# Optimization experiments

Hardware: AMD Instinct MI355X
Metric: run time of the kernel (lower is better)

The kernel has to match this reference:

```python
import jax, jax.numpy as jnp
import numpy as np

S, L, D, H = 4, 2048, 1024, 16
DH = D // H
W_CLUSTER = 384
ROUTING_ITERS = 1
TTOT = S * L


def setup_inputs() -> dict:
    key = jax.random.key(0)
    ks = jax.random.split(key, 8)
    scale = 1.0 / np.sqrt(D)
    return {
        "q_in": jax.random.normal(ks[0], (TTOT, D), jnp.float32),
        "k_in": jax.random.normal(ks[1], (TTOT, D), jnp.float32),
        "v_in": jax.random.normal(ks[2], (TTOT, D), jnp.float32),
        "seqlens_tokens": jnp.full((S,), L, jnp.int32),
        "global_idx_per_set": jax.random.randint(ks[3], (S,), 0, TTOT),
        "Wq": jax.random.normal(ks[4], (D, D), jnp.float32) * scale,
        "Wk": jax.random.normal(ks[5], (D, D), jnp.float32) * scale,
        "Wv": jax.random.normal(ks[6], (D, D), jnp.float32) * scale,
        "Wo": jax.random.normal(ks[7], (D, D), jnp.float32) * scale,
    }


def _l2n(x, eps=1e-6):
    return x / (jnp.linalg.norm(x, axis=-1, keepdims=True) + eps)


def _route_np(r, lens, gidx, w, iters):
    # Host-side per-sequence k-means routing (mirrors the original host-sync loop).
    # Returns augmented token order (global token appended per cluster) and cluster lens.
    bounds = np.concatenate([[0], np.cumsum(lens)])
    order_chunks, len_chunks = [], []
    for s in range(len(lens)):
        a, b = int(bounds[s]), int(bounds[s + 1])
        Ls = b - a
        if Ls <= 0:
            continue
        feats = r[a:b]
        wloc = max(1, min(w, Ls))
        k = max(1, (Ls + wloc - 1) // wloc)
        init_idx = np.clip(np.round(np.linspace(0.0, max(Ls - 1, 0), k)).astype(np.int64), 0, Ls - 1)
        cent = feats[init_idx]
        for _ in range(max(1, iters)):
            sims = feats @ cent.T
            assign = sims.argmax(1)
            sums = np.zeros_like(cent)
            np.add.at(sums, assign, feats)
            counts = np.bincount(assign, minlength=k).astype(cent.dtype)
            cent = sums / np.maximum(counts, 1.0)[:, None]
            cent = cent / (np.linalg.norm(cent, axis=-1, keepdims=True) + 1e-6)
        sims = feats @ cent.T
        assign = sims.argmax(1)
        own = sims[np.arange(Ls), assign]
        order1 = np.argsort(-own, kind="stable")
        assign1 = assign[order1]
        order2 = np.argsort(assign1, kind="stable")
        perm = order1[order2]
        cid = assign1[order2]
        counts = np.bincount(cid, minlength=k)
        keep = np.minimum(counts, wloc)
        starts = np.cumsum(counts) - counts
        pos = np.arange(Ls) - np.repeat(starts, counts)
        keep_mask = pos < keep[cid]
        kept = perm[keep_mask] + a  # absolute kept token indices, cluster-sorted
        kc = keep[keep > 0]
        C = kc.size
        ins = np.cumsum(kc) + np.arange(C)  # insertion slot after each cluster
        total = int(kc.sum()) + C
        wg = np.empty(total, dtype=np.int64)
        m = np.ones(total, dtype=bool)
        m[ins] = False
        wg[m] = kept
        wg[~m] = int(gidx[s])
        order_chunks.append(wg)
        len_chunks.append((kc + 1).astype(np.int64))
    return np.concatenate(order_chunks), np.concatenate(len_chunks)


def _padded_indices(order, lens):
    Ncl, Lmax = lens.size, int(lens.max())
    valid = np.arange(Lmax)[None, :] < lens[:, None]
    idx = np.zeros((Ncl, Lmax), dtype=np.int64)
    idx[valid] = order  # row-major fill matches per-cluster concat order
    return idx, valid


def _attend_and_merge(qh, kh, vh, idx, mask):
    # Padded-varlen non-causal attention per cluster, then mean-merge duplicates.
    scale = 1.0 / np.sqrt(DH)
    qg, kg, vg = qh[idx], kh[idx], vh[idx]  # [Ncl, Lmax, H, Dh]
    scores = jnp.einsum("clhd,cmhd->chlm", qg, kg) * scale
    scores = jnp.where(mask[:, None, None, :], scores, -1e9)
    attn = jax.nn.softmax(scores, axis=-1)
    out = jnp.einsum("chlm,cmhd->clhd", attn, vg)
    out = out * mask[:, :, None, None]
    out_h = jnp.zeros((TTOT, H, DH), out.dtype).at[idx].add(out)
    cnt = jnp.zeros((TTOT,), out.dtype).at[idx].add(mask.astype(out.dtype))
    return out_h / jnp.clip(cnt, 1.0)[:, None, None]


def reference(q_in, k_in, v_in, seqlens_tokens, global_idx_per_set, Wq, Wk, Wv, Wo):
    qh = (q_in @ Wq.T).reshape(TTOT, H, DH)
    kh = (k_in @ Wk.T).reshape(TTOT, H, DH)
    vh = (v_in @ Wv.T).reshape(TTOT, H, DH)
    r = 0.5 * (_l2n(qh.mean(1)) + _l2n(kh.mean(1)))  # routing features (detached in original)
    order, lens = _route_np(np.asarray(r), np.asarray(seqlens_tokens),
                            np.asarray(global_idx_per_set), W_CLUSTER, ROUTING_ITERS)
    idx_np, valid_np = _padded_indices(order, lens)
    idx, mask = jnp.asarray(idx_np), jnp.asarray(valid_np)
    out_h = _attend_and_merge(qh, kh, vh, idx, mask)
    return out_h.reshape(TTOT, D) @ Wo.T
```

## Files before the change

kernel.cpp:

```cpp
#include <hip/hip_runtime.h>
#include <math.h>

#define S_ 4
#define L_ 2048
#define D_ 1024
#define H_ 16
#define DH_ 64
#define TTOT_ 8192
#define WCL_ 384
#define KMAX_ 16
#define MAXCL_ (S_*KMAX_)
#define MAXLEN_ (WCL_+1)
#define LSCAP_ 4096
#define NELEM_ ((size_t)TTOT_*(size_t)D_)

typedef __attribute__((ext_vector_type(8))) short bf16x8;
typedef __attribute__((ext_vector_type(4))) float f32x4;
typedef __attribute__((ext_vector_type(4))) unsigned short u16x4;

__device__ __forceinline__ unsigned short bfh(float x) {
  unsigned u = __float_as_uint(x);
  return (unsigned short)((u + 0x7FFFu + ((u >> 16) & 1u)) >> 16);
}
__device__ __forceinline__ float bff(unsigned short h) {
  return __uint_as_float(((unsigned)h) << 16);
}
__device__ __forceinline__ unsigned pk2(unsigned short a, unsigned short b) {
  return (unsigned)a | ((unsigned)b << 16);
}
#define SWZ(r, c) (((r) << 6) + ((c) ^ (((r) & 7) << 3)))

__device__ __forceinline__ void glds16(const void* g, void* l) {
  __builtin_amdgcn_global_load_lds(
      (const __attribute__((address_space(1))) unsigned int*)g,
      (__attribute__((address_space(3))) unsigned int*)l, 16, 0, 0);
}

#define N4W_ ((1 << 20) / 4)
#define N4IN_ ((int)(NELEM_ / 4))
#define NWM_ (64 * 1024)

__global__ __launch_bounds__(256)
void wmean2(const float* __restrict__ Wq, const float* __restrict__ Wk,
            float* __restrict__ Wqm, float* __restrict__ Wkm) {
  const float* __restrict__ W = blockIdx.y ? Wk : Wq;
  float* __restrict__ Wm = blockIdx.y ? Wkm : Wqm;
  int i = blockIdx.x * 256 + threadIdx.x;
  if (i >= NWM_) return;
  int d = i >> 10, kk = i & 1023;
  float s = 0.f;
#pragma unroll
  for (int h = 0; h < 16; h++) s += W[(size_t)(h * 64 + d) * 1024 + kk];
  Wm[i] = s * (1.0f / 16.0f);
}

__global__ __launch_bounds__(256)
void feats_conv(const float* __restrict__ q_in, const float* __restrict__ k_in,
                const float* __restrict__ v_in,
                const float* __restrict__ Wqm, const float* __restrict__ Wkm,
                float* __restrict__ FQ, float* __restrict__ FK,
                const float* __restrict__ Wq, const float* __restrict__ Wk,
                const float* __restrict__ Wv, const float* __restrict__ Wo,
                unsigned short* __restrict__ WqH, unsigned short* __restrict__ WkH,
                unsigned short* __restrict__ WvH, unsigned short* __restrict__ WoH,
                unsigned short* __restrict__ QSh, unsigned short* __restrict__ KSh,
                unsigned short* __restrict__ VSh) {
  if (blockIdx.x < 256) {
    const int by = blockIdx.x >> 7;
    const float* __restrict__ A = by ? k_in : q_in;
    const float* __restrict__ B = by ? Wkm : Wqm;
    float* __restrict__ C = by ? FK : FQ;
    const int Kd = 1024, N = 64;
    __shared__ float As[16][68];
    __shared__ float Bs[16][68];
    const int tx = threadIdx.x & 15, ty = threadIdx.x >> 4;
    const int m0 = (blockIdx.x & 127) * 64;
    const int lr = threadIdx.x >> 2, lc = threadIdx.x & 3;
    float acc[4][4] = {};
    for (int k0 = 0; k0 < Kd; k0 += 16) {
      __syncthreads();
      float4 a4 = *(const float4*)(A + (size_t)(m0 + lr) * Kd + k0 + lc * 4);
      float4 b4 = *(const float4*)(B + (size_t)lr * Kd + k0 + lc * 4);
      As[lc*4+0][lr] = a4.x; As[lc*4+1][lr] = a4.y; As[lc*4+2][lr] = a4.z; As[lc*4+3][lr] = a4.w;
      Bs[lc*4+0][lr] = b4.x; Bs[lc*4+1][lr] = b4.y; Bs[lc*4+2][lr] = b4.z; Bs[lc*4+3][lr] = b4.w;
      __syncthreads();
#pragma unroll
      for (int kk = 0; kk < 16; kk++) {
        float4 av = *(const float4*)&As[kk][ty * 4];
        float4 bv = *(const float4*)&Bs[kk][tx * 4];
        float aa[4] = {av.x, av.y, av.z, av.w};
        float bb[4] = {bv.x, bv.y, bv.z, bv.w};
#pragma unroll
        for (int i = 0; i < 4; i++)
#pragma unroll
          for (int j = 0; j < 4; j++) acc[i][j] += aa[i] * bb[j];
      }
    }
#pragma unroll
    for (int i = 0; i < 4; i++)
#pragma unroll
      for (int j = 0; j < 4; j++)
        C[(size_t)(m0 + ty * 4 + i) * N + (tx * 4 + j)] = acc[i][j];
    return;
  }
  int i = (blockIdx.x - 256) * 256 + threadIdx.x;
  if (i < 4 * N4W_) {
    int w = i / N4W_, j = i % N4W_;
    const float* src = (w == 0) ? Wq : (w == 1) ? Wk : (w == 2) ? Wv : Wo;
    unsigned short* dst = (w == 0) ? WqH : (w == 1) ? WkH : (w == 2) ? WvH : WoH;
    float4 v = ((const float4*)src)[j];
    *(uint2*)&dst[(size_t)j * 4] =
        make_uint2(pk2(bfh(v.x), bfh(v.y)), pk2(bfh(v.z), bfh(v.w)));
    return;
  }
  i -= 4 * N4W_;
  if (i >= 3 * N4IN_) return;
  int w = i / N4IN_, j = i % N4IN_;
  const float* src = (w == 0) ? q_in : (w == 1) ? k_in : v_in;
  unsigned short* dh = (w == 0) ? QSh : (w == 1) ? KSh : VSh;
  float4 v = ((const float4*)src)[j];
  *(uint2*)&dh[(size_t)j * 4] =
      make_uint2(pk2(bfh(v.x), bfh(v.y)), pk2(bfh(v.z), bfh(v.w)));
}

__device__ __forceinline__
void gemm1_body(const unsigned short* __restrict__ Ah,
                const unsigned short* __restrict__ Bh,
                unsigned short* __restrict__ Ch,
                int b, unsigned char* smem) {
  const int Kd = D_, N = D_;
  const int m0 = (b & 63) * 128, n0 = (b >> 6) * 128;
  unsigned short* LA = (unsigned short*)smem;
  unsigned short* LB = LA + 8192;
  const int tid = threadIdx.x, wave = tid >> 6, lane = tid & 63;
  const int lm = lane & 15, lg = lane >> 4;
  const int wr = wave >> 1, wc = wave & 1;
  const int lrow = lane >> 3;
  const int lchk = (lane & 7) ^ lrow;
  f32x4 acc[4][4];
#pragma unroll
  for (int i = 0; i < 4; i++)
#pragma unroll
    for (int j = 0; j < 4; j++) acc[i][j] = (f32x4){0.f, 0.f, 0.f, 0.f};
  for (int k0 = 0; k0 < Kd; k0 += 64) {
    __syncthreads();
#pragma unroll
    for (int i = 0; i < 4; i++) {
      const int r = wave * 32 + i * 8;
      const size_t ga = (size_t)(m0 + r + lrow) * Kd + k0 + lchk * 8;
      const size_t gb = (size_t)(n0 + r + lrow) * Kd + k0 + lchk * 8;
      glds16(&Ah[ga], &LA[r * 64]);
      glds16(&Bh[gb], &LB[r * 64]);
    }
    __syncthreads();
#pragma unroll
    for (int s = 0; s < 2; s++) {
      bf16x8 ah[4], bh[4];
#pragma unroll
      for (int i = 0; i < 4; i++) {
        const int ra = wr * 64 + i * 16 + lm;
        const int ca = ((s * 4 + lg) ^ (ra & 7)) * 8;
        ah[i] = *(const bf16x8*)&LA[ra * 64 + ca];
        const int rb = wc * 64 + i * 16 + lm;
        const int cb = ((s * 4 + lg) ^ (rb & 7)) * 8;
        bh[i] = *(const bf16x8*)&LB[rb * 64 + cb];
      }
#pragma unroll
      for (int i = 0; i < 4; i++)
#pragma unroll
        for (int j = 0; j < 4; j++)
          acc[i][j] = __builtin_amdgcn_mfma_f32_16x16x32_bf16(ah[i], bh[j], acc[i][j], 0, 0, 0);
    }
  }
#pragma unroll
  for (int i = 0; i < 4; i++)
#pragma unroll
    for (int j = 0; j < 4; j++) {
      const int rowb = m0 + wr * 64 + i * 16 + lg * 4;
      const int col = n0 + wc * 64 + j * 16 + lm;
#pragma unroll
      for (int r = 0; r < 4; r++)
        Ch[(size_t)(rowb + r) * N + col] = bfh(acc[i][j][r]);
    }
}

__global__ __launch_bounds__(256)
void gemm_o1(const unsigned short* __restrict__ Ah,
             const unsigned short* __restrict__ Bh,
             float* __restrict__ C) {
  __shared__ __align__(16) unsigned short LA[128 * 64];
  __shared__ __align__(16) unsigned short LB[128 * 64];
  const int Kd = D_, N = D_;
  const int tid = threadIdx.x, wave = tid >> 6, lane = tid & 63;
  const int lm = lane & 15, lg = lane >> 4;
  const int m0 = (blockIdx.x & 63) * 128, n0 = (blockIdx.x >> 6) * 128;
  const int wr = wave >> 1, wc = wave & 1;
  const int lrow = lane >> 3;
  const int lchk = (lane & 7) ^ lrow;
  f32x4 acc[4][4];
#pragma unroll
  for (int i = 0; i < 4; i++)
#pragma unroll
    for (int j = 0; j < 4; j++) acc[i][j] = (f32x4){0.f, 0.f, 0.f, 0.f};
  for (int k0 = 0; k0 < Kd; k0 += 64) {
    __syncthreads();
#pragma unroll
    for (int i = 0; i < 4; i++) {
      const int r = wave * 32 + i * 8;
      const size_t ga = (size_t)(m0 + r + lrow) * Kd + k0 + lchk * 8;
      const size_t gb = (size_t)(n0 + r + lrow) * Kd + k0 + lchk * 8;
      glds16(&Ah[ga], &LA[r * 64]);
      glds16(&Bh[gb], &LB[r * 64]);
    }
    __syncthreads();
#pragma unroll
    for (int s = 0; s < 2; s++) {
      bf16x8 ah[4], bh[4];
#pragma unroll
      for (int i = 0; i < 4; i++) {
        const int ra = wr * 64 + i * 16 + lm;
        const int ca = ((s * 4 + lg) ^ (ra & 7)) * 8;
        ah[i] = *(const bf16x8*)&LA[ra * 64 + ca];
        const int rb = wc * 64 + i * 16 + lm;
        const int cb = ((s * 4 + lg) ^ (rb & 7)) * 8;
        bh[i] = *(const bf16x8*)&LB[rb * 64 + cb];
      }
#pragma unroll
      for (int i = 0; i < 4; i++)
#pragma unroll
        for (int j = 0; j < 4; j++)
          acc[i][j] = __builtin_amdgcn_mfma_f32_16x16x32_bf16(ah[i], bh[j], acc[i][j], 0, 0, 0);
    }
  }
#pragma unroll
  for (int i = 0; i < 4; i++)
#pragma unroll
    for (int j = 0; j < 4; j++) {
      const int rowb = m0 + wr * 64 + i * 16 + lg * 4;
      const int col = n0 + wc * 64 + j * 16 + lm;
#pragma unroll
      for (int r = 0; r < 4; r++)
        C[(size_t)(rowb + r) * N + col] = acc[i][j][r];
    }
}

__global__ __launch_bounds__(256)
void l2comb(const float* __restrict__ FQ, const float* __restrict__ FK,
            float* __restrict__ FE) {
  int t = blockIdx.x * 4 + (threadIdx.x >> 6);
  int lane = threadIdx.x & 63;
  if (t >= TTOT_) return;
  float q = FQ[(size_t)t * 64 + lane], k = FK[(size_t)t * 64 + lane];
  float q2 = q * q, k2 = k * k;
#pragma unroll
  for (int m = 1; m < 64; m <<= 1) {
    q2 += __shfl_xor(q2, m, 64);
    k2 += __shfl_xor(k2, m, 64);
  }
  FE[(size_t)t * 64 + lane] =
      0.5f * (q / (sqrtf(q2) + 1e-6f) + k / (sqrtf(k2) + 1e-6f));
}

__device__ void routing_body(int s, const float* __restrict__ FE,
                             const int* __restrict__ seqlens,
                             const int* __restrict__ gidx, int* __restrict__ cT,
                             int* __restrict__ cL, int* __restrict__ tC,
                             unsigned char* smem) {
  __builtin_amdgcn_s_setprio(1);
  unsigned long long* keys = (unsigned long long*)smem;
  unsigned char* assign = smem + 32768;
  float (*cent)[64] = (float(*)[64])(smem + 36864);
  int* cnt1 = (int*)(smem + 40960);
  int* cnt2 = cnt1 + KMAX_;
  int* starts = cnt2 + KMAX_;
  float* fstage = (float*)smem;

  const int tid = threadIdx.x;
  int a = 0;
  for (int t = 0; t < s; t++) a += seqlens[t];
  int Ls = seqlens[s];
  if (Ls > LSCAP_) Ls = LSCAP_;
  for (int cs = tid; cs < KMAX_; cs += 1024) cL[s * KMAX_ + cs] = 0;
  if (Ls <= 0) return;

  int wloc = Ls < WCL_ ? Ls : WCL_;
  if (wloc < 1) wloc = 1;
  int k = (Ls + wloc - 1) / wloc;
  if (k < 1) k = 1;
  if (k > KMAX_) k = KMAX_;

  if (tid < k * 64) {
    int j = tid >> 6, d = tid & 63;
    double step = (k > 1) ? (double)(Ls - 1) / (double)(k - 1) : 0.0;
    long ii = (long)rint(step * (double)j);
    if (ii < 0) ii = 0;
    if (ii > Ls - 1) ii = Ls - 1;
    cent[j][d] = FE[(size_t)(a + ii) * DH_ + d];
  }
  if (tid < KMAX_) { cnt1[tid] = 0; cnt2[tid] = 0; }
  __syncthreads();

  for (int base2 = 0; base2 < Ls; base2 += 1024) {
    int i = base2 + tid;
    int aj = -1;
    if (i < Ls) {
      const float4* f4 = (const float4*)(FE + (size_t)(a + i) * DH_);
      float4 fr[16];
#pragma unroll
      for (int c4 = 0; c4 < 16; c4++) fr[c4] = f4[c4];
      float best = -1e30f; int bj = 0;
      for (int j = 0; j < k; j++) {
        float sd = 0.f;
#pragma unroll
        for (int c4 = 0; c4 < 16; c4++) {
          float4 cv = *(const float4*)&cent[j][c4 * 4];
          sd += fr[c4].x * cv.x; sd += fr[c4].y * cv.y;
          sd += fr[c4].z * cv.z; sd += fr[c4].w * cv.w;
        }
        if (sd > best) { best = sd; bj = j; }
      }
      assign[i] = (unsigned char)bj;
      aj = bj;
    }
    for (int j = 0; j < k; j++) {
      unsigned long long m = __ballot(aj == j);
      if ((tid & 63) == 0 && m) atomicAdd(&cnt1[j], (int)__popcll(m));
    }
  }
  __syncthreads();

  float csum_acc = 0.f;
  const int jj = tid >> 6, dd = tid & 63;
  for (int base = 0; base < Ls; base += 128) {
    const int cr = (Ls - base < 128) ? (Ls - base) : 128;
    __syncthreads();
#pragma unroll
    for (int f = tid; f < 128 * 16; f += 1024) {
      int row = f >> 4;
      if (row < cr)
        ((float4*)fstage)[f] =
            *(const float4*)(FE + (size_t)(a + base + row) * DH_ + (f & 15) * 4);
    }
    __syncthreads();
    if (jj < k) {
      const float* fp = fstage + dd;
      int i = 0;
      for (; i + 16 <= cr; i += 16) {
        float v[16];
#pragma unroll
        for (int u = 0; u < 16; u++) v[u] = fp[(i + u) * DH_];
        unsigned char aa[16];
#pragma unroll
        for (int u = 0; u < 16; u++) aa[u] = assign[base + i + u];
#pragma unroll
        for (int u = 0; u < 16; u++)
          csum_acc += (aa[u] == (unsigned char)jj) ? v[u] : 0.0f;
      }
      for (; i < cr; i++)
        csum_acc += (assign[base + i] == (unsigned char)jj) ? fp[i * DH_] : 0.0f;
    }
  }
  __syncthreads();
  if (tid < k * 64) {
    float v = csum_acc / fmaxf((float)cnt1[jj], 1.0f);
    float sq = v * v;
#pragma unroll
    for (int m = 1; m < 64; m <<= 1) sq += __shfl_xor(sq, m, 64);
    cent[jj][dd] = v / (sqrtf(sq) + 1e-6f);
  }
  __syncthreads();

  int NP2 = 1;
  while (NP2 < Ls) NP2 <<= 1;
  for (int base2 = 0; base2 < NP2; base2 += 1024) {
    int i = base2 + tid;
    int aj = -1;
    if (i < NP2) {
      unsigned long long key;
      if (i < Ls) {
        const float4* f4 = (const float4*)(FE + (size_t)(a + i) * DH_);
        float4 fr[16];
#pragma unroll
        for (int c4 = 0; c4 < 16; c4++) fr[c4] = f4[c4];
        float best = -1e30f; int bj = 0;
        for (int j = 0; j < k; j++) {
          float sd = 0.f;
#pragma unroll
          for (int c4 = 0; c4 < 16; c4++) {
            float4 cv = *(const float4*)&cent[j][c4 * 4];
            sd += fr[c4].x * cv.x; sd += fr[c4].y * cv.y;
            sd += fr[c4].z * cv.z; sd += fr[c4].w * cv.w;
          }
          if (sd > best) { best = sd; bj = j; }
        }
        aj = bj;
        unsigned int u = __float_as_uint(best);
        unsigned int ord = (u & 0x80000000u) ? ~u : (u | 0x80000000u);
        unsigned int dsc = ~ord;
        key = ((unsigned long long)bj << 45) |
              ((unsigned long long)dsc << 13) | (unsigned long long)i;
      } else {
        key = ~0ull;
      }
      keys[i] = key;
    }
    for (int j = 0; j < k; j++) {
      unsigned long long m = __ballot(aj == j);
      if ((tid & 63) == 0 && m) atomicAdd(&cnt2[j], (int)__popcll(m));
    }
  }
  __syncthreads();

  for (int len2 = 2; len2 <= NP2; len2 <<= 1) {
    for (int st = len2 >> 1; st > 0; st >>= 1) {
      if (st >= 64) {
        __syncthreads();
      } else {
        asm volatile("s_waitcnt lgkmcnt(0)" ::: "memory");
      }
      for (int i = tid; i < NP2; i += 1024) {
        int j = i ^ st;
        if (j > i) {
          unsigned long long x = keys[i], y = keys[j];
          bool asc = ((i & len2) == 0);
          if ((x > y) == asc) { keys[i] = y; keys[j] = x; }
        }
      }
    }
  }
  __syncthreads();
  if (tid == 0) {
    starts[0] = 0;
    for (int j = 0; j < k; j++) starts[j + 1] = starts[j] + cnt2[j];
  }
  __syncthreads();

  const int g = gidx[s];
  int cOut = 0;
  for (int j = 0; j < k; j++) {
    int cj = cnt2[j];
    if (cj <= 0) continue;
    int keep = cj < wloc ? cj : wloc;
    int slot = s * KMAX_ + cOut;
    for (int p = tid; p < keep; p += 1024) {
      int token = a + (int)(keys[starts[j] + p] & 0x1FFFull);
      cT[slot * MAXLEN_ + p] = token;
      atomicAdd(&tC[token], 1);
    }
    if (tid == 0) {
      cT[slot * MAXLEN_ + keep] = g;
      atomicAdd(&tC[g], 1);
      cL[slot] = keep + 1;
    }
    cOut++;
  }
}

__global__ __launch_bounds__(1024)
void fused_qkvr(const unsigned short* __restrict__ QAh,
                const unsigned short* __restrict__ WqH,
                unsigned short* __restrict__ Qh,
                const unsigned short* __restrict__ KAh,
                const unsigned short* __restrict__ WkH,
                unsigned short* __restrict__ Kh,
                const unsigned short* __restrict__ VAh,
                const unsigned short* __restrict__ WvH,
                unsigned short* __restrict__ Vh,
                const float* __restrict__ FE, const int* __restrict__ seqlens,
                const int* __restrict__ gidx, int* __restrict__ cT,
                int* __restrict__ cL, int* __restrict__ tC) {
  __shared__ __align__(16) unsigned char smem[49152];
  if (blockIdx.x < 4) {
    routing_body(blockIdx.x, FE, seqlens, gidx, cT, cL, tC, smem);
    return;
  }
  if (threadIdx.x >= 256) return;
  int b = blockIdx.x - 4;
  if (b < 512) {
    gemm1_body(QAh, WqH, Qh, b, smem);
  } else if (b < 1024) {
    gemm1_body(KAh, WkH, Kh, b - 512, smem);
  } else {
    gemm1_body(VAh, WvH, Vh, b - 1024, smem);
  }
}

__global__ __launch_bounds__(256)
void attn_kernel(const unsigned short* __restrict__ Qh,
                 const unsigned short* __restrict__ Kh,
                 const unsigned short* __restrict__ Vh,
                 const int* __restrict__ cT, const int* __restrict__ cL,
                 float* __restrict__ OH) {
  const int flat = blockIdx.x;
  const int xcd = flat & 7;
  const int i8 = flat >> 3;
  const int qc = i8 % 7;
  const int g = xcd + 8 * (i8 / 7);
  const int h = g & 15, c = g >> 4;

  const int len = cL[c];
  const int q0 = qc * 64;
  if (len <= 0 || q0 >= len) return;

  __shared__ int toks[MAXLEN_];
  __shared__ __align__(16) unsigned short QP[4096];
  __shared__ __align__(16) unsigned short KT[4096];
  __shared__ __align__(16) unsigned short VT[4096];

  const int tid = threadIdx.x, wave = tid >> 6, lane = tid & 63;
  const int lm = lane & 15, lg = lane >> 4;
  const int lr8 = lane >> 3;
  const int lc8 = (lane & 7) ^ lr8;

  const int krow = tid >> 2;
  const int kc = (tid & 3) * 16;
  const int dg = tid & 15, kg = tid >> 4;
  const int vd0 = dg * 4;

  for (int i = tid; i < len; i += 256) toks[i] = cT[c * MAXLEN_ + i];
  __syncthreads();

  uint4 ka0, ka1;
  u16x4 va0, va1, va2, va3;

#define KV_LOAD(mt_) do {                                                      \
    int kr_ = (mt_) * 64 + krow;                                               \
    int tk_ = toks[kr_ < len ? kr_ : 0];                                       \
    const unsigned short* kph = Kh + (size_t)tk_ * D_ + h * DH_ + kc;          \
    ka0 = *(const uint4*)(kph);  ka1 = *(const uint4*)(kph + 8);               \
    int vr_ = (mt_) * 64 + kg * 4;                                             \
    int t0_ = toks[vr_ + 0 < len ? vr_ + 0 : 0];                               \
    int t1_ = toks[vr_ + 1 < len ? vr_ + 1 : 0];                               \
    int t2_ = toks[vr_ + 2 < len ? vr_ + 2 : 0];                               \
    int t3_ = toks[vr_ + 3 < len ? vr_ + 3 : 0];                               \
    size_t off_ = (size_t)h * DH_ + vd0;                                       \
    va0 = *(const u16x4*)(Vh + (size_t)t0_ * D_ + off_);                       \
    va1 = *(const u16x4*)(Vh + (size_t)t1_ * D_ + off_);                       \
    va2 = *(const u16x4*)(Vh + (size_t)t2_ * D_ + off_);                       \
    va3 = *(const u16x4*)(Vh + (size_t)t3_ * D_ + off_);                       \
  } while (0)

#define KV_WRITE() do {                                                        \
    *(uint4*)&KT[SWZ(krow, kc)] = ka0;                                         \
    *(uint4*)&KT[SWZ(krow, kc + 8)] = ka1;                                     \
    _Pragma("unroll") for (int dd = 0; dd < 4; dd++) {                         \
      *(uint2*)&VT[SWZ(vd0 + dd, kg * 4)] =                                    \
          make_uint2(pk2(va0[dd], va1[dd]), pk2(va2[dd], va3[dd]));            \
    }                                                                          \
  } while (0)

#pragma unroll
  for (int i = 0; i < 2; i++) {
    int slab = wave * 2 + i;
    int r8 = slab * 8;
    int row = q0 + r8 + lr8;
    int tok = toks[row < len ? row : 0];
    glds16(Qh + (size_t)tok * D_ + h * DH_ + lc8 * 8, &QP[r8 * 64]);
  }
  KV_LOAD(0);
  __syncthreads();

  bf16x8 qAh[2];
#pragma unroll
  for (int s = 0; s < 2; s++)
    qAh[s] = *(const bf16x8*)&QP[SWZ(wave * 16 + lm, s * 32 + lg * 8)];

  f32x4 accO[4];
#pragma unroll
  for (int t = 0; t < 4; t++) accO[t] = (f32x4){0.f, 0.f, 0.f, 0.f};
  float mm[4] = {-INFINITY, -INFINITY, -INFINITY, -INFINITY};
  float ll[4] = {0.f, 0.f, 0.f, 0.f};

  const int ntile = (len + 63) >> 6;
  for (int mt = 0; mt < ntile; mt++) {
    __syncthreads();
    KV_WRITE();
    __syncthreads();
    if (mt + 1 < ntile) KV_LOAD(mt + 1);

    f32x4 sA[4];
#pragma unroll
    for (int t = 0; t < 4; t++) sA[t] = (f32x4){0.f, 0.f, 0.f, 0.f};
    __builtin_amdgcn_s_setprio(1);
#pragma unroll
    for (int t = 0; t < 4; t++) {
#pragma unroll
      for (int s = 0; s < 2; s++) {
        bf16x8 kb = *(const bf16x8*)&KT[SWZ(t * 16 + lm, s * 32 + lg * 8)];
        sA[t] = __builtin_amdgcn_mfma_f32_16x16x32_bf16(qAh[s], kb, sA[t], 0, 0, 0);
      }
    }
    __builtin_amdgcn_s_setprio(0);

    float sc[4][4];
#pragma unroll
    for (int t = 0; t < 4; t++) {
      bool kvalid = (mt * 64 + t * 16 + lm) < len;
#pragma unroll
      for (int r = 0; r < 4; r++)
        sc[t][r] = kvalid ? sA[t][r] * 0.125f : -1e9f;
    }
    float mx[4], nn[4], cor[4], sum[4];
#pragma unroll
    for (int r = 0; r < 4; r++) {
      mx[r] = fmaxf(fmaxf(sc[0][r], sc[1][r]), fmaxf(sc[2][r], sc[3][r]));
      mx[r] = fmaxf(mx[r], __shfl_xor(mx[r], 1, 64));
      mx[r] = fmaxf(mx[r], __shfl_xor(mx[r], 2, 64));
      mx[r] = fmaxf(mx[r], __shfl_xor(mx[r], 4, 64));
      mx[r] = fmaxf(mx[r], __shfl_xor(mx[r], 8, 64));
      nn[r] = fmaxf(mm[r], mx[r]);
      cor[r] = __expf(mm[r] - nn[r]);
      mm[r] = nn[r];
    }
    float pp[4][4];
#pragma unroll
    for (int t = 0; t < 4; t++)
#pragma unroll
      for (int r = 0; r < 4; r++) pp[t][r] = __expf(sc[t][r] - nn[r]);
#pragma unroll
    for (int r = 0; r < 4; r++) {
      sum[r] = (pp[0][r] + pp[1][r]) + (pp[2][r] + pp[3][r]);
      sum[r] += __shfl_xor(sum[r], 1, 64);
      sum[r] += __shfl_xor(sum[r], 2, 64);
      sum[r] += __shfl_xor(sum[r], 4, 64);
      sum[r] += __shfl_xor(sum[r], 8, 64);
      ll[r] = ll[r] * cor[r] + sum[r];
    }
#pragma unroll
    for (int t = 0; t < 4; t++) {
#pragma unroll
      for (int r = 0; r < 4; r++) {
        accO[t][r] *= cor[r];
        int row = wave * 16 + lg * 4 + r, col = t * 16 + lm;
        QP[SWZ(row, col)] = bfh(pp[t][r]);
      }
    }

    bf16x8 pAh[2];
#pragma unroll
    for (int s = 0; s < 2; s++)
      pAh[s] = *(const bf16x8*)&QP[SWZ(wave * 16 + lm, s * 32 + lg * 8)];
    __builtin_amdgcn_s_setprio(1);
#pragma unroll
    for (int t = 0; t < 4; t++) {
#pragma unroll
      for (int s = 0; s < 2; s++) {
        bf16x8 vb = *(const bf16x8*)&VT[SWZ(t * 16 + lm, s * 32 + lg * 8)];
        accO[t] = __builtin_amdgcn_mfma_f32_16x16x32_bf16(pAh[s], vb, accO[t], 0, 0, 0);
      }
    }
    __builtin_amdgcn_s_setprio(0);
  }
#undef KV_LOAD
#undef KV_WRITE

#pragma unroll
  for (int t = 0; t < 4; t++) {
#pragma unroll
    for (int r = 0; r < 4; r++) {
      int row = q0 + wave * 16 + lg * 4 + r;
      if (row < len)
        atomicAdd(&OH[(size_t)toks[row] * D_ + h * DH_ + t * 16 + lm],
                  accO[t][r] / ll[r]);
    }
  }
}

__global__ __launch_bounds__(256)
void norm_h(const float* __restrict__ OH, const int* __restrict__ cnt,
            unsigned short* __restrict__ oh) {
  size_t i = (size_t)blockIdx.x * 256 + threadIdx.x;
  size_t n4 = NELEM_ / 4;
  if (i >= n4) return;
  int row = (int)((i * 4) >> 10);
  int cc = cnt[row];
  float s = 1.0f / (float)(cc > 1 ? cc : 1);
  float4 v = ((const float4*)OH)[i];
  v.x *= s; v.y *= s; v.z *= s; v.w *= s;
  *(uint2*)&oh[i * 4] =
      make_uint2(pk2(bfh(v.x), bfh(v.y)), pk2(bfh(v.z), bfh(v.w)));
}

extern "C" void kernel_launch(void* const* d_in, const int* in_sizes, int n_in,
                              void* d_out, int out_size, void* d_ws, size_t ws_size,
                              hipStream_t stream) {
  (void)in_sizes; (void)n_in; (void)out_size; (void)ws_size;
  const float* q_in = (const float*)d_in[0];
  const float* k_in = (const float*)d_in[1];
  const float* v_in = (const float*)d_in[2];
  const int* seqlens = (const int*)d_in[3];
  const int* gidx    = (const int*)d_in[4];
  const float* Wq = (const float*)d_in[5];
  const float* Wk = (const float*)d_in[6];
  const float* Wv = (const float*)d_in[7];
  const float* Wo = (const float*)d_in[8];
  float* out = (float*)d_out;

  unsigned short* Qh = (unsigned short*)d_ws;
  unsigned short* Ql = Qh + NELEM_;
  unsigned short* Kh = Ql + NELEM_;
  unsigned short* Kl = Kh + NELEM_;
  unsigned short* Vh = Kl + NELEM_;
  unsigned short* Vl = Vh + NELEM_;
  float* OH = (float*)(Vl + NELEM_);
  float* WS = OH + NELEM_;
  float* FE = WS + (4 << 19);
  float* FQ = FE + (size_t)TTOT_ * DH_;
  float* FK = FQ + (size_t)TTOT_ * DH_;
  float* Wqm = FK + (size_t)TTOT_ * DH_;
  float* Wkm = Wqm + 64 * 1024;
  int* cT = (int*)(Wkm + 64 * 1024);
  int* cL = cT + MAXCL_ * MAXLEN_;
  int* tC = cL + MAXCL_;

  unsigned short* QSh = (unsigned short*)OH;
  unsigned short* KSh = (unsigned short*)out;
  unsigned short* VSh = Kl;
  unsigned short* WqH = (unsigned short*)WS;
  unsigned short* WkH = WqH + (1 << 20);
  unsigned short* WvH = WkH + (1 << 20);
  unsigned short* WoH = WvH + (1 << 20);
  unsigned short* OHh = Qh;

  hipMemsetAsync(tC, 0, TTOT_ * sizeof(int), stream);

  wmean2<<<dim3(256, 2), 256, 0, stream>>>(Wq, Wk, Wqm, Wkm);

  feats_conv<<<256 + (4 * N4W_ + 3 * N4IN_ + 255) / 256, 256, 0, stream>>>(
      q_in, k_in, v_in, Wqm, Wkm, FQ, FK,
      Wq, Wk, Wv, Wo, WqH, WkH, WvH, WoH, QSh, KSh, VSh);

  l2comb<<<TTOT_ / 4, 256, 0, stream>>>(FQ, FK, FE);

  fused_qkvr<<<4 + 1536, 1024, 0, stream>>>(QSh, WqH, Qh,
                                            KSh, WkH, Kh,
                                            VSh, WvH, Vh,
                                            FE, seqlens, gidx, cT, cL, tC);

  hipMemsetAsync(OH, 0, NELEM_ * sizeof(float), stream);
  attn_kernel<<<7 * H_ * MAXCL_, 256, 0, stream>>>(
      Qh, Kh, Vh, cT, cL, OH);

  norm_h<<<(unsigned)((NELEM_ / 4 + 255) / 256), 256, 0, stream>>>(OH, tC, OHh);
  gemm_o1<<<512, 256, 0, stream>>>(OHh, WoH, out);
}
```

Measured before the change: 304.1 us.

## Fuse count normalization into output GEMM and fold OH zeroing into QKV kernel

The standalone norm_h pass is removed. The output projection GEMM now reads the fp32 attention accumulator directly, scales each row by its inverse cluster count, converts to bf16 and writes it into LDS. The memset of the accumulator moves into extra blocks of the fused QKV/routing kernel, and the staging buffer for Q moves from OH to Vl so OH can be zeroed there. This drops one launch and a full fp32 read plus bf16 write round trip. In exchange the GEMM A-operand loads become synchronous fp32 register loads instead of async global-to-LDS copies, which doubles A-side bytes per GEMM.

New measurement: 299.1 us. About the same (-1.7%).

```diff
diff --git a/kernel.cpp b/kernel.cpp
--- a/kernel.cpp
+++ b/kernel.cpp
@@ -185,7 +185,7 @@
 }
 
 __global__ __launch_bounds__(256)
-void gemm_o1(const unsigned short* __restrict__ Ah,
+void gemm_on(const float* __restrict__ OHf, const int* __restrict__ cnt,
              const unsigned short* __restrict__ Bh,
              float* __restrict__ C) {
   __shared__ __align__(16) unsigned short LA[128 * 64];
@@ -207,9 +207,19 @@
 #pragma unroll
     for (int i = 0; i < 4; i++) {
       const int r = wave * 32 + i * 8;
-      const size_t ga = (size_t)(m0 + r + lrow) * Kd + k0 + lchk * 8;
+      const int arow = m0 + r + lrow;
+      const float* asrc = OHf + (size_t)arow * Kd + k0 + lchk * 8;
+      float4 a0 = *(const float4*)asrc;
+      float4 a1 = *(const float4*)(asrc + 4);
+      int cc = cnt[arow];
+      float sc = 1.0f / (float)(cc > 1 ? cc : 1);
+      uint4 pk;
+      pk.x = pk2(bfh(a0.x * sc), bfh(a0.y * sc));
+      pk.y = pk2(bfh(a0.z * sc), bfh(a0.w * sc));
+      pk.z = pk2(bfh(a1.x * sc), bfh(a1.y * sc));
+      pk.w = pk2(bfh(a1.z * sc), bfh(a1.w * sc));
+      *(uint4*)&LA[r * 64 + lane * 8] = pk;
       const size_t gb = (size_t)(n0 + r + lrow) * Kd + k0 + lchk * 8;
-      glds16(&Ah[ga], &LA[r * 64]);
       glds16(&Bh[gb], &LB[r * 64]);
     }
     __syncthreads();
@@ -466,6 +476,7 @@
                 const unsigned short* __restrict__ VAh,
                 const unsigned short* __restrict__ WvH,
                 unsigned short* __restrict__ Vh,
+                float* __restrict__ OHz,
                 const float* __restrict__ FE, const int* __restrict__ seqlens,
                 const int* __restrict__ gidx, int* __restrict__ cT,
                 int* __restrict__ cL, int* __restrict__ tC) {
@@ -474,8 +485,13 @@
     routing_body(blockIdx.x, FE, seqlens, gidx, cT, cL, tC, smem);
     return;
   }
+  int b = blockIdx.x - 4;
+  if (b >= 1536) {
+    size_t o = (size_t)(b - 1536) * 1024 + threadIdx.x;
+    ((float4*)OHz)[o] = (float4){0.f, 0.f, 0.f, 0.f};
+    return;
+  }
   if (threadIdx.x >= 256) return;
-  int b = blockIdx.x - 4;
   if (b < 512) {
     gemm1_body(QAh, WqH, Qh, b, smem);
   } else if (b < 1024) {
@@ -666,21 +682,6 @@
   }
 }
 
-__global__ __launch_bounds__(256)
-void norm_h(const float* __restrict__ OH, const int* __restrict__ cnt,
-            unsigned short* __restrict__ oh) {
-  size_t i = (size_t)blockIdx.x * 256 + threadIdx.x;
-  size_t n4 = NELEM_ / 4;
-  if (i >= n4) return;
-  int row = (int)((i * 4) >> 10);
-  int cc = cnt[row];
-  float s = 1.0f / (float)(cc > 1 ? cc : 1);
-  float4 v = ((const float4*)OH)[i];
-  v.x *= s; v.y *= s; v.z *= s; v.w *= s;
-  *(uint2*)&oh[i * 4] =
-      make_uint2(pk2(bfh(v.x), bfh(v.y)), pk2(bfh(v.z), bfh(v.w)));
-}
-
 extern "C" void kernel_launch(void* const* d_in, const int* in_sizes, int n_in,
                               void* d_out, int out_size, void* d_ws, size_t ws_size,
                               hipStream_t stream) {
@@ -713,14 +714,13 @@
   int* cL = cT + MAXCL_ * MAXLEN_;
   int* tC = cL + MAXCL_;
 
-  unsigned short* QSh = (unsigned short*)OH;
+  unsigned short* QSh = Vl;
   unsigned short* KSh = (unsigned short*)out;
   unsigned short* VSh = Kl;
   unsigned short* WqH = (unsigned short*)WS;
   unsigned short* WkH = WqH + (1 << 20);
   unsigned short* WvH = WkH + (1 << 20);
   unsigned short* WoH = WvH + (1 << 20);
-  unsigned short* OHh = Qh;
 
   hipMemsetAsync(tC, 0, TTOT_ * sizeof(int), stream);
 
@@ -732,15 +732,14 @@
 
   l2comb<<<TTOT_ / 4, 256, 0, stream>>>(FQ, FK, FE);
 
-  fused_qkvr<<<4 + 1536, 1024, 0, stream>>>(QSh, WqH, Qh,
-                                            KSh, WkH, Kh,
-                                            VSh, WvH, Vh,
-                                            FE, seqlens, gidx, cT, cL, tC);
-
-  hipMemsetAsync(OH, 0, NELEM_ * sizeof(float), stream);
+  fused_qkvr<<<4 + 1536 + 2048, 1024, 0, stream>>>(QSh, WqH, Qh,
+                                                   KSh, WkH, Kh,
+                                                   VSh, WvH, Vh,
+                                                   OH,
+                                                   FE, seqlens, gidx, cT, cL, tC);
+
   attn_kernel<<<7 * H_ * MAXCL_, 256, 0, stream>>>(
       Qh, Kh, Vh, cT, cL, OH);
 
-  norm_h<<<(unsigned)((NELEM_ / 4 + 255) / 256), 256, 0, stream>>>(OH, tC, OHh);
-  gemm_o1<<<512, 256, 0, stream>>>(OHh, WoH, out);
-}
+  gemm_on<<<512, 256, 0, stream>>>(OH, tC, WoH, out);
+}
```
